# Performance work log

Measured on AMD Instinct MI355X. Metric: run time of the kernel, lower is better.

Reference implementation:

```python
import jax, jax.numpy as jnp
import numpy as np

THETA = 10000.0  # RoPE base


def _rope(x):
    # x: [B, T, H] with H even. Matches torch view_as_complex on (..., H//2, 2)
    # pairing of adjacent elements, rotated by m * theta_i.
    B, T, H = x.shape
    inv_freq = 1.0 / (THETA ** (jnp.arange(0, H, 2, dtype=jnp.float32) / H))  # [H/2]
    ang = jnp.arange(T, dtype=jnp.float32)[:, None] * inv_freq[None, :]       # [T, H/2]
    cos, sin = jnp.cos(ang), jnp.sin(ang)
    xr = x.astype(jnp.float32).reshape(B, T, H // 2, 2)
    a, b = xr[..., 0], xr[..., 1]
    out = jnp.stack([a * cos - b * sin, a * sin + b * cos], axis=-1)          # complex mult
    return out.reshape(B, T, H).astype(x.dtype)


def setup_inputs() -> dict:
    key = jax.random.key(0)
    k1, k2, k3, k4 = jax.random.split(key, 4)
    B, T, C, H = 4, 4096, 1024, 64
    return {
        "x": jax.random.normal(k1, (B, T, C), dtype=jnp.float32),
        "wq": jax.random.normal(k2, (C, H), dtype=jnp.float32) * 0.02,
        "wk": jax.random.normal(k3, (C, H), dtype=jnp.float32) * 0.02,
        "wv": jax.random.normal(k4, (C, H), dtype=jnp.float32) * 0.02,
    }


def reference(x, wq, wk, wv):
    # Head.forward, training branch; dropout is identity (eval determinism).
    B, T, C = x.shape
    H = wq.shape[1]
    q = _rope(x @ wq)   # [B, T, H]
    k = _rope(x @ wk)   # [B, T, H]
    v = x @ wv          # [B, T, H]
    wei = jnp.einsum('bqh,bkh->bqk', q, k) * (H ** -0.5)   # [B, T, T]
    causal = jnp.tril(jnp.ones((T, T), dtype=bool))
    wei = jnp.where(causal, wei, -jnp.inf)
    wei = jax.nn.softmax(wei, axis=-1)
    out = jnp.einsum('bqk,bkh->bqh', wei, v)               # [B, T, H]
    return out
```

## Files before the change

### kernel.cpp

```cpp
#include <hip/hip_runtime.h>
#include <hip/hip_bf16.h>
#include <math.h>

#define B_ 4
#define T_ 4096
#define C_ 1024
#define H_ 64
#define ROWS_ (B_*T_)

typedef __attribute__((ext_vector_type(8))) short bf16x8;
typedef __attribute__((ext_vector_type(4))) float f32x4;

__device__ __forceinline__ unsigned short f2bf(float f) {
    union { float f; unsigned u; } x; x.f = f;
    unsigned r = x.u + 0x7fffu + ((x.u >> 16) & 1u);
    return (unsigned short)(r >> 16);
}
__device__ __forceinline__ float bf2f(unsigned short s) {
    union { unsigned u; float f; } x; x.u = ((unsigned)s) << 16;
    return x.f;
}
__device__ __forceinline__ unsigned pk2bf(float a, float b) {
    __hip_bfloat162 h = __float22bfloat162_rn(float2{a, b});
    return *reinterpret_cast<unsigned*>(&h);
}
__device__ __forceinline__ void gld16(const void* g, void* l) {
    __builtin_amdgcn_global_load_lds(
        (const __attribute__((address_space(1))) unsigned*)g,
        (__attribute__((address_space(3))) unsigned*)l, 16, 0, 0);
}

__global__ __launch_bounds__(256) void prep_kernel(
    const float* __restrict__ wq, const float* __restrict__ wk,
    const float* __restrict__ wv, unsigned short* __restrict__ wt,
    float* __restrict__ tab)
{
    __shared__ float ts[64][68];
    const int tid = threadIdx.x;
    if (blockIdx.x < 48) {
        const int m  = blockIdx.x >> 4;
        const int k0 = (blockIdx.x & 15) * 64;
        const float* w = (m == 0) ? wq : (m == 1) ? wk : wv;
        {
            const int r = tid >> 2;
            const int c = (tid & 3) * 16;
            #pragma unroll
            for (int i = 0; i < 4; ++i)
                *reinterpret_cast<float4*>(&ts[r][c + 4*i]) =
                    *reinterpret_cast<const float4*>(&w[(size_t)(k0 + r)*H_ + c + 4*i]);
        }
        __syncthreads();
        {
            const int n  = tid >> 2;
            const int kc = (tid & 3) * 16;
            unsigned short outp[16];
            #pragma unroll
            for (int j = 0; j < 16; ++j) outp[j] = f2bf(ts[kc + j][n]);
            unsigned short* dst = &wt[((size_t)m*64 + n)*C_ + k0 + kc];
            *reinterpret_cast<uint4*>(dst)     = *reinterpret_cast<uint4*>(&outp[0]);
            *reinterpret_cast<uint4*>(dst + 8) = *reinterpret_cast<uint4*>(&outp[8]);
        }
    } else {
        const int idx = (blockIdx.x - 48)*256 + tid;
        const int t   = idx >> 5;
        const int hp  = idx & 31;
        const float inv = __builtin_exp2f(-(float)hp * (13.287712379549449f / 32.f));
        float sn, cs;
        sincosf((float)t * inv, &sn, &cs);
        *reinterpret_cast<float2*>(&tab[2*idx]) = float2{cs, sn};
    }
}

__global__ __launch_bounds__(512, 2) void qkv_mfma_kernel(
    const float* __restrict__ x, const unsigned short* __restrict__ wt,
    const float* __restrict__ tab,
    unsigned short* __restrict__ qb, unsigned short* __restrict__ kb,
    unsigned short* __restrict__ vtb)
{
    __shared__ unsigned short SM[32768];

    const int tid  = threadIdx.x;
    const int w    = tid >> 6;
    const int lane = tid & 63;
    const int rt   = w >> 1;
    const int ch   = w & 1;
    const int lr   = lane & 15;
    const int lg   = lane >> 4;
    const int rb   = blockIdx.x * 64;

    const int ar = tid >> 3;
    const int ac = (tid & 7) * 8;

    float4 axr[2];

    auto load_A = [&](int t) {
        const float* p = &x[(size_t)(rb + ar)*C_ + t*64 + ac];
        axr[0] = *reinterpret_cast<const float4*>(p);
        axr[1] = *reinterpret_cast<const float4*>(p + 4);
    };
    auto write_A = [&](int buf) {
        unsigned tmp[4];
        tmp[0] = pk2bf(axr[0].x, axr[0].y);
        tmp[1] = pk2bf(axr[0].z, axr[0].w);
        tmp[2] = pk2bf(axr[1].x, axr[1].y);
        tmp[3] = pk2bf(axr[1].z, axr[1].w);
        const int off = buf*8192 + ar*128 + ((ac*2) ^ ((ar & 7) << 4));
        *reinterpret_cast<uint4*>((char*)SM + off) = *reinterpret_cast<uint4*>(tmp);
    };
    auto stage_W = [&](int t, int buf) {
        #pragma unroll
        for (int s = 0; s < 3; ++s) {
            const int slot = s*512 + tid;
            const int r    = slot >> 3;
            const int c8   = (slot & 7) * 8;
            const int c8s  = c8 ^ ((r & 7) << 3);
            gld16(&wt[(size_t)r*C_ + t*64 + c8s],
                  (char*)SM + 16384 + buf*24576 + slot*16);
        }
    };

    f32x4 acc[6];
    #pragma unroll
    for (int j = 0; j < 6; ++j) acc[j] = f32x4{0.f, 0.f, 0.f, 0.f};

    load_A(0);
    stage_W(0, 0);
    write_A(0);
    load_A(1);

    for (int t = 0; t < 16; ++t) {
        const int cur = t & 1, nxt = cur ^ 1;
        __syncthreads();
        if (t < 15) { stage_W(t + 1, nxt); write_A(nxt); }
        if (t < 14) load_A(t + 2);
        char* Acur = (char*)SM + cur*8192;
        char* Wcur = (char*)SM + 16384 + cur*24576;
        #pragma unroll
        for (int kh = 0; kh < 2; ++kh) {
            const int arow = rt*16 + lr;
            bf16x8 af = *reinterpret_cast<const bf16x8*>(
                Acur + arow*128 + ((kh*64 + lg*16) ^ ((arow & 7) << 4)));
            #pragma unroll
            for (int j = 0; j < 6; ++j) {
                const int n = ch*96 + j*16 + lr;
                bf16x8 bf = *reinterpret_cast<const bf16x8*>(
                    Wcur + n*128 + ((kh*64 + lg*16) ^ ((n & 7) << 4)));
                acc[j] = __builtin_amdgcn_mfma_f32_16x16x32_bf16(af, bf, acc[j], 0, 0, 0);
            }
        }
    }

    __syncthreads();
    const int rl0  = rt*16 + lg*4;
    const int row0 = rb + rl0;
    #pragma unroll
    for (int j = 0; j < 6; ++j) {
        const int c = ch*96 + j*16 + lr;
        const int m = c >> 6;
        const int h = c & 63;
        if (m < 2) {
            const int base_ls = (m == 0) ? 0 : 4096;
            const float qs = (m == 0) ? 0.125f : 1.0f;
            const int hp = h >> 1;
            #pragma unroll
            for (int i = 0; i < 4; ++i) {
                const float v  = acc[j][i];
                const float pr = __shfl_xor(v, 1);
                if (!(h & 1)) {
                    const int tp = (row0 + i) & (T_ - 1);
                    const float2 cssn = *reinterpret_cast<const float2*>(
                        &tab[((size_t)tp*32 + hp)*2]);
                    const float oe = (v*cssn.x - pr*cssn.y) * qs;
                    const float oo = (v*cssn.y + pr*cssn.x) * qs;
                    *reinterpret_cast<unsigned*>(&SM[base_ls + (rl0 + i)*64 + h]) =
                        pk2bf(oe, oo);
                }
            }
        } else {
            unsigned short pk[4];
            #pragma unroll
            for (int i = 0; i < 4; ++i) pk[i] = f2bf(acc[j][i]);
            char* vbase = (char*)SM + 16384 + h*128;
            *reinterpret_cast<uint2*>(vbase + ((rl0*2) ^ ((h & 7) << 3))) =
                *reinterpret_cast<uint2*>(pk);
        }
    }
    __syncthreads();
    {
        const int row = tid >> 3;
        const int h0  = (tid & 7) * 8;
        *reinterpret_cast<uint4*>(&qb[(size_t)(rb + row)*H_ + h0]) =
            *reinterpret_cast<const uint4*>(&SM[row*64 + h0]);
        *reinterpret_cast<uint4*>(&kb[(size_t)(rb + row)*H_ + h0]) =
            *reinterpret_cast<const uint4*>(&SM[4096 + row*64 + h0]);
        const int h  = tid >> 3;
        const int t0 = (tid & 7) * 8;
        char* vbase = (char*)SM + 16384 + h*128;
        uint2 a  = *reinterpret_cast<uint2*>(vbase + (((t0*2)    ) ^ ((h & 7) << 3)));
        uint2 b2 = *reinterpret_cast<uint2*>(vbase + (((t0*2) + 8) ^ ((h & 7) << 3)));
        const int bh  = (rb >> 12)*64 + h;
        const int tp0 = rb & (T_ - 1);
        uint4 o; o.x = a.x; o.y = a.y; o.z = b2.x; o.w = b2.y;
        *reinterpret_cast<uint4*>(&vtb[(size_t)bh*T_ + tp0 + t0]) = o;
    }
}

__global__ __launch_bounds__(256, 3) void attn_chunk_kernel(
    const unsigned short* __restrict__ qb, const unsigned short* __restrict__ kb,
    const unsigned short* __restrict__ vtb,
    unsigned short* __restrict__ partO, float* __restrict__ partML,
    int CH, int per_batch)
{
    __shared__ unsigned short Kls[2][4096];
    __shared__ unsigned short Vls[2][4096];
    __shared__ unsigned short Pls[4][2048];

    const int tid  = threadIdx.x;
    const int w    = tid >> 6;
    const int lane = tid & 63;
    const int lr   = lane & 15;
    const int lg   = lane >> 4;

    const int cid = blockIdx.x;
    const int b   = cid / per_batch;
    int r0 = cid - b*per_batch;
    const int G = CH >> 1;
    int a = 0, off = 0;
    while (r0 >= off + G*(a + 1)) { off += G*(a + 1); ++a; }
    const int idx = r0 - off;
    const int qt  = G*a + idx/(a + 1);
    const int c   = idx % (a + 1);

    const int q0  = qt * 128;
    const int kt0 = c * CH;
    const int ntk = 2*qt + 2;
    const int ns  = min(kt0 + CH, ntk) - kt0;
    const size_t rbase = (size_t)b * T_;
    const int dtile = 2*qt + (w >> 1);

    char* Pw = (char*)&Pls[w][0];

    bf16x8 qf[2][2];
    #pragma unroll
    for (int s16 = 0; s16 < 2; ++s16) {
        const unsigned short* qp = qb + (rbase + q0 + w*32 + s16*16 + lr)*H_ + lg*8;
        qf[s16][0] = *reinterpret_cast<const bf16x8*>(qp);
        qf[s16][1] = *reinterpret_cast<const bf16x8*>(qp + 32);
    }

    float mrow[2] = {-1e30f, -1e30f};
    float lrow[2] = {0.f, 0.f};
    f32x4 acc[2][4];
    #pragma unroll
    for (int s16 = 0; s16 < 2; ++s16)
        #pragma unroll
        for (int hs = 0; hs < 4; ++hs) acc[s16][hs] = f32x4{0.f, 0.f, 0.f, 0.f};

    const int srow = tid >> 3;
    const int scol = (tid & 7) * 8;
    auto stage_dma = [&](int kt, int buf) {
        #pragma unroll
        for (int s = 0; s < 2; ++s) {
            const int r    = s*32 + srow;
            const int c8s  = scol ^ ((r & 7) << 3);
            const int slot = s*256 + tid;
            gld16(&kb[(rbase + (size_t)kt*64 + r)*H_ + c8s],
                  (char*)&Kls[buf][0] + slot*16);
            gld16(&vtb[((size_t)(b*64 + r))*T_ + (size_t)kt*64 + c8s],
                  (char*)&Vls[buf][0] + slot*16);
        }
    };

    stage_dma(kt0, 0);

    for (int s = 0; s < ns; ++s) {
        __syncthreads();
        if (s + 1 < ns) stage_dma(kt0 + s + 1, (s + 1) & 1);
        const int kt = kt0 + s;
        char* Kb = (char*)&Kls[s & 1][0];
        char* Vb = (char*)&Vls[s & 1][0];

        if (kt <= dtile) {
            f32x4 st[2][4];
            __builtin_amdgcn_s_setprio(1);
            #pragma unroll
            for (int ks = 0; ks < 4; ++ks) {
                const int rr2 = ks*16 + lr;
                const int sw  = (rr2 & 7) << 4;
                bf16x8 kf0 = *reinterpret_cast<const bf16x8*>(Kb + rr2*128 + ((lg*16     ) ^ sw));
                bf16x8 kf1 = *reinterpret_cast<const bf16x8*>(Kb + rr2*128 + ((lg*16 + 64) ^ sw));
                #pragma unroll
                for (int s16 = 0; s16 < 2; ++s16) {
                    f32x4 t = {0.f, 0.f, 0.f, 0.f};
                    t = __builtin_amdgcn_mfma_f32_16x16x32_bf16(kf0, qf[s16][0], t, 0, 0, 0);
                    t = __builtin_amdgcn_mfma_f32_16x16x32_bf16(kf1, qf[s16][1], t, 0, 0, 0);
                    st[s16][ks] = t;
                }
            }
            __builtin_amdgcn_s_setprio(0);

            float scl[2];
            const int swp = (lr & 7) << 4;
            #pragma unroll
            for (int s16 = 0; s16 < 2; ++s16) {
                const int qg = q0 + w*32 + s16*16 + lr;
                float mx = -1e30f;
                if (kt == dtile) {
                    #pragma unroll
                    for (int ks = 0; ks < 4; ++ks)
                        #pragma unroll
                        for (int i = 0; i < 4; ++i) {
                            const int kg = kt*64 + ks*16 + lg*4 + i;
                            const float v = (kg <= qg) ? st[s16][ks][i] : -1e30f;
                            st[s16][ks][i] = v;
                            mx = fmaxf(mx, v);
                        }
                } else {
                    #pragma unroll
                    for (int ks = 0; ks < 4; ++ks)
                        #pragma unroll
                        for (int i = 0; i < 4; ++i) mx = fmaxf(mx, st[s16][ks][i]);
                }
                mx = fmaxf(mx, __shfl_xor(mx, 16));
                mx = fmaxf(mx, __shfl_xor(mx, 32));
                const float mn = fmaxf(mrow[s16], mx);
                scl[s16] = __expf(mrow[s16] - mn);
                float ls = 0.f;
                #pragma unroll
                for (int ks = 0; ks < 4; ++ks)
                    #pragma unroll
                    for (int i = 0; i < 4; ++i) {
                        const float p = __expf(st[s16][ks][i] - mn);
                        st[s16][ks][i] = p;
                        ls += p;
                    }
                ls += __shfl_xor(ls, 16);
                ls += __shfl_xor(ls, 32);
                lrow[s16] = lrow[s16]*scl[s16] + ls;
                mrow[s16] = mn;

                const int pr = s16*16 + lr;
                #pragma unroll
                for (int ks = 0; ks < 4; ++ks) {
                    const unsigned u0 = pk2bf(st[s16][ks][0], st[s16][ks][1]);
                    const unsigned u1 = pk2bf(st[s16][ks][2], st[s16][ks][3]);
                    *reinterpret_cast<uint2*>(Pw + pr*128 + ((ks*32 + lg*8) ^ swp)) =
                        make_uint2(u0, u1);
                }
            }

            #pragma unroll
            for (int s16 = 0; s16 < 2; ++s16) {
                float sclr[4];
                #pragma unroll
                for (int i = 0; i < 4; ++i) sclr[i] = __shfl(scl[s16], lg*4 + i);
                #pragma unroll
                for (int hs = 0; hs < 4; ++hs)
                    #pragma unroll
                    for (int i = 0; i < 4; ++i) acc[s16][hs][i] *= sclr[i];
            }

            bf16x8 pf[2][2];
            #pragma unroll
            for (int s16 = 0; s16 < 2; ++s16) {
                const int pr = s16*16 + lr;
                pf[s16][0] = *reinterpret_cast<const bf16x8*>(Pw + pr*128 + ((lg*16     ) ^ swp));
                pf[s16][1] = *reinterpret_cast<const bf16x8*>(Pw + pr*128 + ((lg*16 + 64) ^ swp));
            }
            __builtin_amdgcn_s_setprio(1);
            #pragma unroll
            for (int hs = 0; hs < 4; ++hs) {
                const int rv  = hs*16 + lr;
                const int swv = (rv & 7) << 4;
                bf16x8 vf0 = *reinterpret_cast<const bf16x8*>(Vb + rv*128 + ((lg*16     ) ^ swv));
                bf16x8 vf1 = *reinterpret_cast<const bf16x8*>(Vb + rv*128 + ((lg*16 + 64) ^ swv));
                #pragma unroll
                for (int s16 = 0; s16 < 2; ++s16) {
                    acc[s16][hs] = __builtin_amdgcn_mfma_f32_16x16x32_bf16(pf[s16][0], vf0, acc[s16][hs], 0, 0, 0);
                    acc[s16][hs] = __builtin_amdgcn_mfma_f32_16x16x32_bf16(pf[s16][1], vf1, acc[s16][hs], 0, 0, 0);
                }
            }
            __builtin_amdgcn_s_setprio(0);
        }
    }

    #pragma unroll
    for (int s16 = 0; s16 < 2; ++s16) {
        const int myrow = w*32 + s16*16 + lr;
        if (lg == 0) {
            partML[(size_t)cid*256 + myrow]       = mrow[s16];
            partML[(size_t)cid*256 + 128 + myrow] = lrow[s16];
        }
    }
    __syncthreads();
    unsigned short* Ols = &Kls[0][0];
    #pragma unroll
    for (int s16 = 0; s16 < 2; ++s16)
        #pragma unroll
        for (int hs = 0; hs < 4; ++hs)
            #pragma unroll
            for (int i = 0; i < 4; ++i)
                Ols[(w*32 + s16*16 + lg*4 + i)*64 + hs*16 + lr] =
                    f2bf(acc[s16][hs][i]);
    __syncthreads();
    {
        const int e0 = tid * 32;
        #pragma unroll
        for (int j = 0; j < 4; ++j)
            *reinterpret_cast<uint4*>(&partO[(size_t)cid*8192 + e0 + 8*j]) =
                *reinterpret_cast<const uint4*>(&Ols[e0 + 8*j]);
    }
}

__global__ __launch_bounds__(256) void combine_kernel(
    const unsigned short* __restrict__ partO, const float* __restrict__ partML,
    float* __restrict__ out, int CH, int per_batch)
{
    const int bq   = blockIdx.x;
    const int b    = bq >> 6;
    const int qt   = (bq >> 1) & 31;
    const int half = bq & 1;
    const int G  = CH >> 1;
    const int a  = qt / G;
    const int nc = a + 1;
    const int cb = b*per_batch + (G*a*(a + 1))/2 + (qt - G*a)*(a + 1);

    const int tid = threadIdx.x;
    const int row = half*64 + (tid >> 2);
    const int h0  = (tid & 3) * 16;

    float mi[8], wi[8];
    float M = -1e30f;
    #pragma unroll
    for (int i = 0; i < 8; ++i) if (i < nc) {
        mi[i] = partML[(size_t)(cb + i)*256 + row];
        M = fmaxf(M, mi[i]);
    }
    float L = 0.f;
    #pragma unroll
    for (int i = 0; i < 8; ++i) if (i < nc) {
        wi[i] = __expf(mi[i] - M);
        L += partML[(size_t)(cb + i)*256 + 128 + row] * wi[i];
    }
    const float inv = 1.f / L;

    float o[16];
    #pragma unroll
    for (int j = 0; j < 16; ++j) o[j] = 0.f;
    #pragma unroll
    for (int i = 0; i < 8; ++i) if (i < nc) {
        const unsigned short* p = &partO[(size_t)(cb + i)*8192 + (size_t)row*64 + h0];
        uint4 u0 = *reinterpret_cast<const uint4*>(p);
        uint4 u1 = *reinterpret_cast<const uint4*>(p + 8);
        const unsigned* uu = (const unsigned*)&u0;
        #pragma unroll
        for (int j = 0; j < 4; ++j) {
            o[2*j]   += bf2f((unsigned short)(uu[j] & 0xffffu)) * wi[i];
            o[2*j+1] += bf2f((unsigned short)(uu[j] >> 16))     * wi[i];
        }
        const unsigned* uv = (const unsigned*)&u1;
        #pragma unroll
        for (int j = 0; j < 4; ++j) {
            o[8+2*j]   += bf2f((unsigned short)(uv[j] & 0xffffu)) * wi[i];
            o[8+2*j+1] += bf2f((unsigned short)(uv[j] >> 16))     * wi[i];
        }
    }
    float* op = &out[((size_t)b*T_ + (size_t)qt*128 + row)*H_ + h0];
    #pragma unroll
    for (int j = 0; j < 4; ++j) {
        float4 v = make_float4(o[4*j]*inv, o[4*j+1]*inv, o[4*j+2]*inv, o[4*j+3]*inv);
        *reinterpret_cast<float4*>(op + 4*j) = v;
    }
}

extern "C" void kernel_launch(void* const* d_in, const int* in_sizes, int n_in,
                              void* d_out, int out_size, void* d_ws, size_t ws_size,
                              hipStream_t stream) {
    const float* x  = (const float*)d_in[0];
    const float* wq = (const float*)d_in[1];
    const float* wk = (const float*)d_in[2];
    const float* wv = (const float*)d_in[3];
    float* out = (float*)d_out;

    unsigned short* qb  = (unsigned short*)d_ws;
    unsigned short* kb  = qb  + (size_t)ROWS_ * H_;
    unsigned short* vtb = kb  + (size_t)ROWS_ * H_;
    unsigned short* wt  = vtb + (size_t)ROWS_ * H_;

    const size_t fixed = (size_t)3*ROWS_*H_*2 + (size_t)3*64*C_*2;
    const size_t need8 = fixed + (size_t)576*8192*2 + (size_t)576*256*4;
    int CH, per_batch;
    if (ws_size >= need8) { CH = 8;  per_batch = 144; }
    else                  { CH = 16; per_batch = 80; }
    const int nblk = 4 * per_batch;

    unsigned short* partO  = wt + (size_t)3*64*C_;
    float*          partML = (float*)(partO + (size_t)nblk*8192);

    float* rope_tab = (float*)partO;

    prep_kernel<<<560, 256, 0, stream>>>(wq, wk, wv, wt, rope_tab);
    qkv_mfma_kernel<<<ROWS_/64, 512, 0, stream>>>(x, wt, rope_tab, qb, kb, vtb);
    attn_chunk_kernel<<<nblk, 256, 0, stream>>>(qb, kb, vtb, partO, partML,
                                                CH, per_batch);
    combine_kernel<<<256, 256, 0, stream>>>(partO, partML, out, CH, per_batch);
}
```

Measured before the change: 74.08 us.

## Use 256-row query tiles with 8 waves and exp2-based softmax

The attention kernel moves from 128-row query tiles with 4 waves to 256-row tiles with 8 waves (512 threads), so each K/V tile staged in shared memory serves twice as many query rows. The chunk-split schedule, the partial-output layout and the combine kernel are rewritten to match. Softmax now uses exp2 with log2(e) folded into the Q scale during the RoPE epilogue, saving a multiply per exponential. The larger blocks give fewer blocks in flight and coarser load balance along the causal triangle, and the bigger partial buffers increase workspace traffic.

```diff
diff --git a/kernel.cpp b/kernel.cpp
--- a/kernel.cpp
+++ b/kernel.cpp
@@ -160,7 +160,7 @@
         const int h = c & 63;
         if (m < 2) {
             const int base_ls = (m == 0) ? 0 : 4096;
-            const float qs = (m == 0) ? 0.125f : 1.0f;
+            const float qs = (m == 0) ? 0.18033688011112042f : 1.0f;
             const int hp = h >> 1;
             #pragma unroll
             for (int i = 0; i < 4; ++i) {
@@ -205,15 +205,13 @@
     }
 }
 
-__global__ __launch_bounds__(256, 3) void attn_chunk_kernel(
+__global__ __launch_bounds__(512, 4) void attn_chunk_kernel(
     const unsigned short* __restrict__ qb, const unsigned short* __restrict__ kb,
     const unsigned short* __restrict__ vtb,
     unsigned short* __restrict__ partO, float* __restrict__ partML,
     int CH, int per_batch)
 {
-    __shared__ unsigned short Kls[2][4096];
-    __shared__ unsigned short Vls[2][4096];
-    __shared__ unsigned short Pls[4][2048];
+    __shared__ unsigned short SM[32768];
 
     const int tid  = threadIdx.x;
     const int w    = tid >> 6;
@@ -223,22 +221,22 @@
 
     const int cid = blockIdx.x;
     const int b   = cid / per_batch;
-    int r0 = cid - b*per_batch;
-    const int G = CH >> 1;
-    int a = 0, off = 0;
-    while (r0 >= off + G*(a + 1)) { off += G*(a + 1); ++a; }
-    const int idx = r0 - off;
-    const int qt  = G*a + idx/(a + 1);
-    const int c   = idx % (a + 1);
-
-    const int q0  = qt * 128;
+    int rem = cid - b*per_batch;
+    int qt = 0, c = 0;
+    for (qt = 0; qt < 16; ++qt) {
+        const int n = (4*qt + 4 + CH - 1) / CH;
+        if (rem < n) { c = rem; break; }
+        rem -= n;
+    }
+
+    const int q0  = qt * 256;
     const int kt0 = c * CH;
-    const int ntk = 2*qt + 2;
+    const int ntk = 4*qt + 4;
     const int ns  = min(kt0 + CH, ntk) - kt0;
     const size_t rbase = (size_t)b * T_;
-    const int dtile = 2*qt + (w >> 1);
-
-    char* Pw = (char*)&Pls[w][0];
+    const int dtile = 4*qt + (w >> 1);
+
+    char* Pw = (char*)SM + 32768 + w*4096;
 
     bf16x8 qf[2][2];
     #pragma unroll
@@ -259,16 +257,11 @@
     const int srow = tid >> 3;
     const int scol = (tid & 7) * 8;
     auto stage_dma = [&](int kt, int buf) {
-        #pragma unroll
-        for (int s = 0; s < 2; ++s) {
-            const int r    = s*32 + srow;
-            const int c8s  = scol ^ ((r & 7) << 3);
-            const int slot = s*256 + tid;
-            gld16(&kb[(rbase + (size_t)kt*64 + r)*H_ + c8s],
-                  (char*)&Kls[buf][0] + slot*16);
-            gld16(&vtb[((size_t)(b*64 + r))*T_ + (size_t)kt*64 + c8s],
-                  (char*)&Vls[buf][0] + slot*16);
-        }
+        const int c8s = scol ^ ((srow & 7) << 3);
+        gld16(&kb[(rbase + (size_t)kt*64 + srow)*H_ + c8s],
+              (char*)SM + buf*8192 + tid*16);
+        gld16(&vtb[((size_t)(b*64 + srow))*T_ + (size_t)kt*64 + c8s],
+              (char*)SM + 16384 + buf*8192 + tid*16);
     };
 
     stage_dma(kt0, 0);
@@ -277,8 +270,8 @@
         __syncthreads();
         if (s + 1 < ns) stage_dma(kt0 + s + 1, (s + 1) & 1);
         const int kt = kt0 + s;
-        char* Kb = (char*)&Kls[s & 1][0];
-        char* Vb = (char*)&Vls[s & 1][0];
+        char* Kb = (char*)SM + (s & 1)*8192;
+        char* Vb = (char*)SM + 16384 + (s & 1)*8192;
 
         if (kt <= dtile) {
             f32x4 st[2][4];
@@ -324,13 +317,13 @@
                 mx = fmaxf(mx, __shfl_xor(mx, 16));
                 mx = fmaxf(mx, __shfl_xor(mx, 32));
                 const float mn = fmaxf(mrow[s16], mx);
-                scl[s16] = __expf(mrow[s16] - mn);
+                scl[s16] = __builtin_exp2f(mrow[s16] - mn);
                 float ls = 0.f;
                 #pragma unroll
                 for (int ks = 0; ks < 4; ++ks)
                     #pragma unroll
                     for (int i = 0; i < 4; ++i) {
-                        const float p = __expf(st[s16][ks][i] - mn);
+                        const float p = __builtin_exp2f(st[s16][ks][i] - mn);
                         st[s16][ks][i] = p;
                         ls += p;
                     }
@@ -388,12 +381,12 @@
     for (int s16 = 0; s16 < 2; ++s16) {
         const int myrow = w*32 + s16*16 + lr;
         if (lg == 0) {
-            partML[(size_t)cid*256 + myrow]       = mrow[s16];
-            partML[(size_t)cid*256 + 128 + myrow] = lrow[s16];
+            partML[(size_t)cid*512 + myrow]       = mrow[s16];
+            partML[(size_t)cid*512 + 256 + myrow] = lrow[s16];
         }
     }
     __syncthreads();
-    unsigned short* Ols = &Kls[0][0];
+    unsigned short* Ols = &SM[0];
     #pragma unroll
     for (int s16 = 0; s16 < 2; ++s16)
         #pragma unroll
@@ -407,7 +400,7 @@
         const int e0 = tid * 32;
         #pragma unroll
         for (int j = 0; j < 4; ++j)
-            *reinterpret_cast<uint4*>(&partO[(size_t)cid*8192 + e0 + 8*j]) =
+            *reinterpret_cast<uint4*>(&partO[(size_t)cid*16384 + e0 + 8*j]) =
                 *reinterpret_cast<const uint4*>(&Ols[e0 + 8*j]);
     }
 }
@@ -418,29 +411,31 @@
 {
     const int bq   = blockIdx.x;
     const int b    = bq >> 6;
-    const int qt   = (bq >> 1) & 31;
-    const int half = bq & 1;
-    const int G  = CH >> 1;
-    const int a  = qt / G;
-    const int nc = a + 1;
-    const int cb = b*per_batch + (G*a*(a + 1))/2 + (qt - G*a)*(a + 1);
+    const int rest = bq & 63;
+    const int qt   = rest >> 2;
+    const int qtr  = rest & 3;
+
+    int pre = 0;
+    for (int j = 0; j < qt; ++j) pre += (4*j + 4 + CH - 1) / CH;
+    const int nc = (4*qt + 4 + CH - 1) / CH;
+    const int cb = b*per_batch + pre;
 
     const int tid = threadIdx.x;
-    const int row = half*64 + (tid >> 2);
+    const int row = qtr*64 + (tid >> 2);
     const int h0  = (tid & 3) * 16;
 
-    float mi[8], wi[8];
+    float mi[16], wi[16];
     float M = -1e30f;
     #pragma unroll
-    for (int i = 0; i < 8; ++i) if (i < nc) {
-        mi[i] = partML[(size_t)(cb + i)*256 + row];
+    for (int i = 0; i < 16; ++i) if (i < nc) {
+        mi[i] = partML[(size_t)(cb + i)*512 + row];
         M = fmaxf(M, mi[i]);
     }
     float L = 0.f;
     #pragma unroll
-    for (int i = 0; i < 8; ++i) if (i < nc) {
-        wi[i] = __expf(mi[i] - M);
-        L += partML[(size_t)(cb + i)*256 + 128 + row] * wi[i];
+    for (int i = 0; i < 16; ++i) if (i < nc) {
+        wi[i] = __builtin_exp2f(mi[i] - M);
+        L += partML[(size_t)(cb + i)*512 + 256 + row] * wi[i];
     }
     const float inv = 1.f / L;
 
@@ -448,8 +443,8 @@
     #pragma unroll
     for (int j = 0; j < 16; ++j) o[j] = 0.f;
     #pragma unroll
-    for (int i = 0; i < 8; ++i) if (i < nc) {
-        const unsigned short* p = &partO[(size_t)(cb + i)*8192 + (size_t)row*64 + h0];
+    for (int i = 0; i < 16; ++i) if (i < nc) {
+        const unsigned short* p = &partO[(size_t)(cb + i)*16384 + (size_t)row*64 + h0];
         uint4 u0 = *reinterpret_cast<const uint4*>(p);
         uint4 u1 = *reinterpret_cast<const uint4*>(p + 8);
         const unsigned* uu = (const unsigned*)&u0;
@@ -465,7 +460,7 @@
             o[8+2*j+1] += bf2f((unsigned short)(uv[j] >> 16))     * wi[i];
         }
     }
-    float* op = &out[((size_t)b*T_ + (size_t)qt*128 + row)*H_ + h0];
+    float* op = &out[((size_t)b*T_ + (size_t)qt*256 + row)*H_ + h0];
     #pragma unroll
     for (int j = 0; j < 4; ++j) {
         float4 v = make_float4(o[4*j]*inv, o[4*j+1]*inv, o[4*j+2]*inv, o[4*j+3]*inv);
@@ -488,20 +483,22 @@
     unsigned short* wt  = vtb + (size_t)ROWS_ * H_;
 
     const size_t fixed = (size_t)3*ROWS_*H_*2 + (size_t)3*64*C_*2;
-    const size_t need8 = fixed + (size_t)576*8192*2 + (size_t)576*256*4;
-    int CH, per_batch;
-    if (ws_size >= need8) { CH = 8;  per_batch = 144; }
-    else                  { CH = 16; per_batch = 80; }
+    auto pb = [](int CH) { int s = 0;
+        for (int qt = 0; qt < 16; ++qt) s += (4*qt + 4 + CH - 1)/CH; return s; };
+    int CH = 4, per_batch = pb(4);
+    if (ws_size < fixed + (size_t)4*per_batch*(16384*2 + 512*4)) {
+        CH = 8; per_batch = pb(8);
+    }
     const int nblk = 4 * per_batch;
 
     unsigned short* partO  = wt + (size_t)3*64*C_;
-    float*          partML = (float*)(partO + (size_t)nblk*8192);
+    float*          partML = (float*)(partO + (size_t)nblk*16384);
 
     float* rope_tab = (float*)partO;
 
     prep_kernel<<<560, 256, 0, stream>>>(wq, wk, wv, wt, rope_tab);
     qkv_mfma_kernel<<<ROWS_/64, 512, 0, stream>>>(x, wt, rope_tab, qb, kb, vtb);
-    attn_chunk_kernel<<<nblk, 256, 0, stream>>>(qb, kb, vtb, partO, partML,
+    attn_chunk_kernel<<<nblk, 512, 0, stream>>>(qb, kb, vtb, partO, partML,
                                                 CH, per_batch);
     combine_kernel<<<256, 256, 0, stream>>>(partO, partML, out, CH, per_batch);
 }
```

After: 85.41 us. 15.3% more time.
